# Performance work log

Measured on AMD Instinct MI355X. Metric: run time of the kernel, lower is better.

The kernel has to match this reference:

```python
import jax, jax.numpy as jnp
import numpy as np

B, S, D, H = 4, 2048, 1024, 16
HD = D // H

def setup_inputs() -> dict:
    key = jax.random.key(0)
    ks = jax.random.split(key, 5)
    x = jax.random.normal(ks[0], (B, S, D), dtype=jnp.float32)
    mask = jnp.ones((B, S), dtype=jnp.int32)
    # torch nn.Linear init scale ~ 1/sqrt(fan_in); use small normal for stability
    qkv_w = jax.random.normal(ks[1], (3 * D, D), dtype=jnp.float32) * (1.0 / np.sqrt(D))
    qkv_b = jax.random.normal(ks[2], (3 * D,), dtype=jnp.float32) * 0.02
    out_w = jax.random.normal(ks[3], (D, D), dtype=jnp.float32) * (1.0 / np.sqrt(D))
    out_b = jax.random.normal(ks[4], (D,), dtype=jnp.float32) * 0.02
    return {"x": x, "mask": mask, "qkv_w": qkv_w, "qkv_b": qkv_b,
            "out_w": out_w, "out_b": out_b}

def reference(x, mask, qkv_w, qkv_b, out_w, out_b):
    b, s, d = x.shape
    scale = np.sqrt(HD).astype(np.float32)
    # qkv projection: torch Linear y = x @ W^T + b
    qkv = x @ qkv_w.T + qkv_b                      # (b, s, 3d)
    qkv = qkv.reshape(b, s, 3, H, HD)
    qkv = jnp.transpose(qkv, (2, 0, 3, 1, 4))      # (3, b, H, s, hd)
    q, k, v = qkv[0], qkv[1], qkv[2]
    scores = jnp.einsum('bhqd,bhkd->bhqk', q, k) / scale  # (b, H, s, s)
    neg_inf = jnp.float32(-jnp.inf)
    causal = jnp.tril(jnp.ones((s, s), dtype=bool))
    scores = jnp.where(causal[None, None], scores, neg_inf)
    key_mask = (mask != 0)[:, None, None, :]       # (b, 1, 1, s)
    scores = jnp.where(key_mask, scores, neg_inf)
    attn = jax.nn.softmax(scores, axis=-1)
    out = jnp.einsum('bhqk,bhkd->bhqd', attn, v)   # (b, H, s, hd)
    out = jnp.transpose(out, (0, 2, 1, 3)).reshape(b, s, d)
    return out @ out_w.T + out_b
```

## Files before the change

### kernel.cpp

```cpp
#include <hip/hip_runtime.h>
#include <stdint.h>
#include <type_traits>

#define BB  4
#define SS  2048
#define DD  1024
#define HH  16
#define HDD 64

typedef __attribute__((ext_vector_type(8))) short s16x8;
typedef __attribute__((ext_vector_type(4))) float f32x4;

__device__ inline short f2bf(float f) {
    union { float f; unsigned int u; } v; v.f = f;
    unsigned int r = (v.u + 0x7fffu + ((v.u >> 16) & 1u)) >> 16;
    return (short)r;
}

__device__ inline float bf2f(short s) {
    union { unsigned int u; float f; } v;
    v.u = ((unsigned int)(unsigned short)s) << 16;
    return v.f;
}

__device__ inline unsigned int pk2(float a, float b) {
    return (unsigned int)(unsigned short)f2bf(a) |
           ((unsigned int)(unsigned short)f2bf(b) << 16);
}

#define GLL(gp, lp) __builtin_amdgcn_global_load_lds( \
    (const __attribute__((address_space(1))) void*)(gp), \
    (__attribute__((address_space(3))) void*)(lp), 16, 0, 0)

__device__ inline void lds_barrier() {
    asm volatile("s_waitcnt lgkmcnt(0)" ::: "memory");
    __builtin_amdgcn_sched_barrier(0);
    __builtin_amdgcn_s_barrier();
    __builtin_amdgcn_sched_barrier(0);
}

__global__ void cvt_all(const float* __restrict__ x, const float* __restrict__ qw,
                        const float* __restrict__ ow, short* __restrict__ dst) {
    const int X_N  = BB * SS * DD;
    const int QW_N = 3 * DD * DD;
    int i = (blockIdx.x * 256 + threadIdx.x) * 8;
    const float* s;
    if (i < X_N)            s = x + i;
    else if (i < X_N + QW_N) s = qw + (i - X_N);
    else                     s = ow + (i - X_N - QW_N);
    const float4* sp = (const float4*)s;
    float4 a = sp[0], b = sp[1];
    s16x8 o;
    o[0]=f2bf(a.x); o[1]=f2bf(a.y); o[2]=f2bf(a.z); o[3]=f2bf(a.w);
    o[4]=f2bf(b.x); o[5]=f2bf(b.y); o[6]=f2bf(b.z); o[7]=f2bf(b.w);
    *(s16x8*)(dst + i) = o;
}

template<int EPI>
__global__ __launch_bounds__(256, 3)
void gemm128tb(const short* __restrict__ A, const short* __restrict__ Bw,
               const float* __restrict__ bias, float* __restrict__ Cf,
               short* __restrict__ Qo, short* __restrict__ Ko, short* __restrict__ Vo,
               int M, int N, int K, int nbx)
{
    __shared__ short lsA[3][128 * 32];
    __shared__ short lsB[3][128 * 32];

    const int tid  = threadIdx.x;
    const int w    = tid >> 6, lane = tid & 63;
    const int quad = lane >> 4, l15 = lane & 15;
    const int wm = w >> 1, wn = w & 1;
    const int cpx = gridDim.x >> 3;
    const int swz = (blockIdx.x & 7) * cpx + (blockIdx.x >> 3);
    const int m0 = (swz / nbx) * 128, n0 = (swz % nbx) * 128;
    const int grow = lane >> 2;
    const int gcol = ((lane & 3) ^ (grow & 3)) * 8;
    const int rsw = (l15 & 3);

    f32x4 acc[4][4] = {};

    auto issue = [&](int kt, int buf) {
#pragma unroll
        for (int jj = 0; jj < 2; ++jj) {
            int c = w * 2 + jj;
            GLL(A + (size_t)(m0 + c * 16 + grow) * K + kt * 32 + gcol,
                &lsA[buf][c * 512]);
        }
#pragma unroll
        for (int jj = 0; jj < 2; ++jj) {
            int c = w * 2 + jj;
            GLL(Bw + (size_t)(n0 + c * 16 + grow) * K + kt * 32 + gcol,
                &lsB[buf][c * 512]);
        }
    };

    const int NT = K >> 5;
    issue(0, 0);
    issue(1, 1);
    int buf = 0;
    for (int t = 0; t < NT; ++t) {
        lds_barrier();
        const int nb2 = (buf + 2 >= 3) ? buf - 1 : buf + 2;
        if (t + 2 < NT) {
            issue(t + 2, nb2);
            asm volatile("s_waitcnt vmcnt(8)" ::: "memory");
        } else if (t + 1 < NT) {
            asm volatile("s_waitcnt vmcnt(4)" ::: "memory");
        } else {
            asm volatile("s_waitcnt vmcnt(0)" ::: "memory");
        }
        __builtin_amdgcn_sched_barrier(0);
        __builtin_amdgcn_s_barrier();
        __builtin_amdgcn_sched_barrier(0);

        s16x8 af[4], bfr[4];
#pragma unroll
        for (int mf = 0; mf < 4; ++mf)
            af[mf] = *(const s16x8*)&lsA[buf][(wm * 64 + mf * 16 + l15) * 32 +
                                             ((quad ^ rsw) * 8)];
#pragma unroll
        for (int nf = 0; nf < 4; ++nf)
            bfr[nf] = *(const s16x8*)&lsB[buf][(wn * 64 + nf * 16 + l15) * 32 +
                                              ((quad ^ rsw) * 8)];

        __builtin_amdgcn_s_setprio(1);
#pragma unroll
        for (int mf = 0; mf < 4; ++mf)
#pragma unroll
            for (int nf = 0; nf < 4; ++nf)
                acc[mf][nf] = __builtin_amdgcn_mfma_f32_16x16x32_bf16(
                                  af[mf], bfr[nf], acc[mf][nf], 0, 0, 0);
        __builtin_amdgcn_s_setprio(0);

        buf = (buf + 1 >= 3) ? 0 : buf + 1;
    }

    if (EPI == 0) {
#pragma unroll
        for (int mf = 0; mf < 4; ++mf) {
            int row = m0 + wm * 64 + mf * 16 + quad * 4;
#pragma unroll
            for (int nf = 0; nf < 4; ++nf) {
                int col = n0 + wn * 64 + nf * 16 + l15;
                float bv = bias[col];
#pragma unroll
                for (int r = 0; r < 4; ++r)
                    Cf[(size_t)(row + r) * N + col] = acc[mf][nf][r] + bv;
            }
        }
    } else {
#pragma unroll
        for (int mf = 0; mf < 4; ++mf) {
            int row = m0 + wm * 64 + mf * 16 + quad * 4;
#pragma unroll
            for (int nf = 0; nf < 4; ++nf) {
                int col = n0 + wn * 64 + nf * 16 + l15;
                float bv = bias[col];
                int sel = col >> 10, h = (col >> 6) & 15, hd = col & 63;
#pragma unroll
                for (int r = 0; r < 4; ++r) {
                    int rr = row + r;
                    int b = rr >> 11, s = rr & 2047;
                    short val = f2bf(acc[mf][nf][r] + bv);
                    if (sel == 0)      Qo[(((size_t)b * HH + h) * SS + s) * HDD + hd] = val;
                    else if (sel == 1) Ko[(((size_t)b * HH + h) * SS + s) * HDD + hd] = val;
                    else               Vo[(((size_t)b * HH + h) * HDD + hd) * SS + s] = val;
                }
            }
        }
    }
}

__global__ __launch_bounds__(256, 2)
void attn_kernel(const short* __restrict__ Q, const short* __restrict__ Kb,
                 const short* __restrict__ Vb, const int* __restrict__ mask,
                 short* __restrict__ O)
{
    __shared__ short lsK[2][64 * 64];
    __shared__ short lsV[2][64 * 64];
    __shared__ short lsP[4][32 * 64];
    __shared__ short lsM[SS];

    const int tid  = threadIdx.x;
    const int w    = tid >> 6, lane = tid & 63;
    const int quad = lane >> 4, l15 = lane & 15;
    const int L  = blockIdx.x + 8 * blockIdx.y;
    const int bx = L >> 6;
    const int bh = (L & 7) * 8 + ((L >> 3) & 7);
    const int b = bh >> 4;
    const size_t baseQK = (size_t)bh * SS * HDD;
    const size_t baseV  = (size_t)bh * HDD * SS;
    const float SC = 0.18033688f;
    const int grow = lane >> 3;
    const int gcol = ((lane & 7) ^ grow) * 8;
    const int l7 = l15 & 7;

    {
        const int4* mp = (const int4*)(mask + b * SS);
        int4 a = mp[tid * 2], c = mp[tid * 2 + 1];
        const short NEG = f2bf(-1e30f);
        s16x8 mo;
        mo[0] = a.x ? (short)0 : NEG; mo[1] = a.y ? (short)0 : NEG;
        mo[2] = a.z ? (short)0 : NEG; mo[3] = a.w ? (short)0 : NEG;
        mo[4] = c.x ? (short)0 : NEG; mo[5] = c.y ? (short)0 : NEG;
        mo[6] = c.z ? (short)0 : NEG; mo[7] = c.w ? (short)0 : NEG;
        *(s16x8*)&lsM[tid * 8] = mo;
    }

    auto issue = [&](int kv0, int buf) {
#pragma unroll
        for (int jj = 0; jj < 2; ++jj) {
            int row = w * 16 + jj * 8 + grow;
            GLL(Kb + baseQK + (size_t)(kv0 + row) * HDD + gcol,
                &lsK[buf][(w * 2 + jj) * 512]);
        }
#pragma unroll
        for (int jj = 0; jj < 2; ++jj) {
            int row = w * 16 + jj * 8 + grow;
            GLL(Vb + baseV + (size_t)row * SS + kv0 + gcol,
                &lsV[buf][(w * 2 + jj) * 512]);
        }
    };

    for (int t = 0; t < 2; ++t) {
        const int qb = t ? bx : (15 - bx);
        const int q0 = qb * 128;
        const int qw0 = q0 + w * 32;

        s16x8 aq[2][2];
#pragma unroll
        for (int s = 0; s < 2; ++s)
#pragma unroll
            for (int ks = 0; ks < 2; ++ks)
                aq[s][ks] = *(const s16x8*)(Q + baseQK +
                    (size_t)(qw0 + s * 16 + l15) * HDD + ks * 32 + quad * 8);

        float m_r[2], l_r[2];
        f32x4 o_acc[2][4] = {};
#pragma unroll
        for (int s = 0; s < 2; ++s) { m_r[s] = -1e30f; l_r[s] = 0.f; }

        const int ntiles = 2 * qb + 2;

        lds_barrier();
        issue(0, 0);

        auto tile = [&](auto CC, int kv0, int buf, int kvn) {
            constexpr bool CAUS = decltype(CC)::value;

            lds_barrier();
            if (kvn >= 0) issue(kvn, buf ^ 1);

            float madd[4][4];
#pragma unroll
            for (int nt = 0; nt < 4; ++nt) {
                uint2 mw4 = *(const uint2*)&lsM[kv0 + nt * 16 + quad * 4];
                madd[nt][0] = bf2f((short)(mw4.x & 0xffff));
                madd[nt][1] = bf2f((short)(mw4.x >> 16));
                madd[nt][2] = bf2f((short)(mw4.y & 0xffff));
                madd[nt][3] = bf2f((short)(mw4.y >> 16));
            }

            if (kvn >= 0) asm volatile("s_waitcnt vmcnt(4)" ::: "memory");
            else          asm volatile("s_waitcnt vmcnt(0)" ::: "memory");
            __builtin_amdgcn_sched_barrier(0);
            __builtin_amdgcn_s_barrier();
            __builtin_amdgcn_sched_barrier(0);

            f32x4 sv[2][4];
#pragma unroll
            for (int s = 0; s < 2; ++s)
#pragma unroll
                for (int nt = 0; nt < 4; ++nt) sv[s][nt] = f32x4{};
#pragma unroll
            for (int ks = 0; ks < 2; ++ks)
#pragma unroll
                for (int nt = 0; nt < 4; ++nt) {
                    s16x8 kf = *(const s16x8*)&lsK[buf][(nt * 16 + l15) * 64 +
                                                       (((ks * 4 + quad) ^ l7) * 8)];
#pragma unroll
                    for (int s = 0; s < 2; ++s)
                        sv[s][nt] = __builtin_amdgcn_mfma_f32_16x16x32_bf16(
                                        kf, aq[s][ks], sv[s][nt], 0, 0, 0);
                }

#pragma unroll
            for (int s = 0; s < 2; ++s) {
                const int qg = qw0 + s * 16 + l15;
#pragma unroll
                for (int nt = 0; nt < 4; ++nt) {
                    const int kg0 = kv0 + nt * 16 + quad * 4;
#pragma unroll
                    for (int r = 0; r < 4; ++r) {
                        float scv = sv[s][nt][r] * SC + madd[nt][r];
                        if (CAUS && kg0 + r > qg) scv = -1e30f;
                        sv[s][nt][r] = scv;
                    }
                }
            }

            float rm[2];
#pragma unroll
            for (int s = 0; s < 2; ++s) {
                float v = fmaxf(fmaxf(fmaxf(sv[s][0][0], sv[s][0][1]),
                                      fmaxf(sv[s][0][2], sv[s][0][3])),
                                fmaxf(fmaxf(sv[s][1][0], sv[s][1][1]),
                                      fmaxf(sv[s][1][2], sv[s][1][3])));
                float v2 = fmaxf(fmaxf(fmaxf(sv[s][2][0], sv[s][2][1]),
                                       fmaxf(sv[s][2][2], sv[s][2][3])),
                                 fmaxf(fmaxf(sv[s][3][0], sv[s][3][1]),
                                       fmaxf(sv[s][3][2], sv[s][3][3])));
                v = fmaxf(v, v2);
                v = fmaxf(v, __shfl_xor(v, 16));
                v = fmaxf(v, __shfl_xor(v, 32));
                rm[s] = v;
            }
            float need = fmaxf(rm[0] - m_r[0], rm[1] - m_r[1]);
            if (!__all(need <= 8.0f)) {
#pragma unroll
                for (int s = 0; s < 2; ++s) {
                    float nm = fmaxf(m_r[s], rm[s]);
                    float al = __builtin_amdgcn_exp2f(m_r[s] - nm);
                    m_r[s] = nm;
                    l_r[s] *= al;
#pragma unroll
                    for (int r = 0; r < 4; ++r) {
                        float alq = __shfl(al, (quad << 2) + r + (lane & 48));
#pragma unroll
                        for (int ht = 0; ht < 4; ++ht)
                            o_acc[s][ht][r] *= alq;
                    }
                }
            }
#pragma unroll
            for (int s = 0; s < 2; ++s) {
                float rs = 0.f;
#pragma unroll
                for (int nt = 0; nt < 4; ++nt)
#pragma unroll
                    for (int r = 0; r < 4; ++r) {
                        float p = __builtin_amdgcn_exp2f(sv[s][nt][r] - m_r[s]);
                        sv[s][nt][r] = p;
                        rs += p;
                    }
                l_r[s] += rs;
            }

            short* lsPw = lsP[w];
#pragma unroll
            for (int s = 0; s < 2; ++s)
#pragma unroll
                for (int nt = 0; nt < 4; ++nt) {
                    uint2 pw;
                    pw.x = pk2(sv[s][nt][0], sv[s][nt][1]);
                    pw.y = pk2(sv[s][nt][2], sv[s][nt][3]);
                    int row = s * 16 + l15;
                    int g8 = (nt * 2 + (quad >> 1)) ^ l7;
                    *(uint2*)&lsPw[row * 64 + (g8 << 3) + ((quad & 1) << 2)] = pw;
                }
            asm volatile("s_waitcnt lgkmcnt(0)" ::: "memory");
            __builtin_amdgcn_sched_barrier(0);

            s16x8 ap[2][2];
#pragma unroll
            for (int s = 0; s < 2; ++s)
#pragma unroll
                for (int k2 = 0; k2 < 2; ++k2)
                    ap[s][k2] = *(const s16x8*)&lsPw[(s * 16 + l15) * 64 +
                                                     (((k2 * 4 + quad) ^ l7) << 3)];
#pragma unroll
            for (int ht = 0; ht < 4; ++ht)
#pragma unroll
                for (int k2 = 0; k2 < 2; ++k2) {
                    s16x8 vf = *(const s16x8*)&lsV[buf][(ht * 16 + l15) * 64 +
                                                        (((k2 * 4 + quad) ^ l7) * 8)];
#pragma unroll
                    for (int s = 0; s < 2; ++s)
                        o_acc[s][ht] = __builtin_amdgcn_mfma_f32_16x16x32_bf16(
                                           ap[s][k2], vf, o_acc[s][ht], 0, 0, 0);
                }
        };

        for (int kt = 0; kt < ntiles; ++kt) {
            const int kvn = (kt + 1 < ntiles) ? (kt + 1) * 64 : -1;
            if (kt >= 2 * qb) tile(std::true_type{},  kt * 64, kt & 1, kvn);
            else              tile(std::false_type{}, kt * 64, kt & 1, kvn);
        }

        const int hcol = (bh & 15) * HDD;
#pragma unroll
        for (int s = 0; s < 2; ++s) {
            float ls = l_r[s];
            ls += __shfl_xor(ls, 16);
            ls += __shfl_xor(ls, 32);
#pragma unroll
            for (int r = 0; r < 4; ++r) {
                float lq = __shfl(ls, (quad << 2) + r + (lane & 48));
                float inv = 1.0f / lq;
                int srow = qw0 + s * 16 + quad * 4 + r;
                size_t base = ((size_t)b * SS + srow) * DD + hcol;
#pragma unroll
                for (int ht = 0; ht < 4; ++ht)
                    O[base + ht * 16 + l15] = f2bf(o_acc[s][ht][r] * inv);
            }
        }
    }
}

extern "C" void kernel_launch(void* const* d_in, const int* in_sizes, int n_in,
                              void* d_out, int out_size, void* d_ws, size_t ws_size,
                              hipStream_t stream) {
    const float* x     = (const float*)d_in[0];
    const int*   mask  = (const int*)d_in[1];
    const float* qkv_w = (const float*)d_in[2];
    const float* qkv_b = (const float*)d_in[3];
    const float* out_w = (const float*)d_in[4];
    const float* out_b = (const float*)d_in[5];
    float* out = (float*)d_out;

    const size_t M1 = (size_t)BB * SS;
    short* ws  = (short*)d_ws;
    short* xb  = ws;
    short* qwb = xb  + M1 * DD;
    short* owb = qwb + (size_t)3 * DD * DD;
    short* Qb  = owb + (size_t)DD * DD;
    short* Kb  = Qb  + M1 * DD;
    short* Vb  = Kb  + M1 * DD;
    short* Ob  = Vb  + M1 * DD;

    cvt_all<<<6144, 256, 0, stream>>>(x, qkv_w, out_w, ws);

    gemm128tb<1><<<1536, 256, 0, stream>>>(xb, qwb, qkv_b, nullptr,
                                           Qb, Kb, Vb, 8192, 3072, 1024, 24);
    attn_kernel<<<dim3(8, BB * HH), 256, 0, stream>>>(Qb, Kb, Vb, mask, Ob);
    gemm128tb<0><<<512, 256, 0, stream>>>(Ob, owb, out_b, out,
                                          nullptr, nullptr, nullptr, 8192, 1024, 1024, 8);
}
```

Before: 284.4 us.

## Double KV tile size to 128 and read mask directly from global memory

The attention kernel now processes 128 keys per tile instead of 64. This halves the number of tile iterations and their barriers and softmax rescale checks per query block. LDS buffers for K and V grow to match, and the V tile uses a new swizzle for the 128-wide rows. The shared-memory mask staging is removed in favour of per-tile int4 loads from global memory, which saves LDS and an init pass but adds global loads in each tile. The larger S fragments raise register pressure and LDS use, which may reduce occupancy at two blocks per SM.

```diff
diff --git a/kernel.cpp b/kernel.cpp
--- a/kernel.cpp
+++ b/kernel.cpp
@@ -15,12 +15,6 @@
     union { float f; unsigned int u; } v; v.f = f;
     unsigned int r = (v.u + 0x7fffu + ((v.u >> 16) & 1u)) >> 16;
     return (short)r;
-}
-
-__device__ inline float bf2f(short s) {
-    union { unsigned int u; float f; } v;
-    v.u = ((unsigned int)(unsigned short)s) << 16;
-    return v.f;
 }
 
 __device__ inline unsigned int pk2(float a, float b) {
@@ -176,10 +170,9 @@
                  const short* __restrict__ Vb, const int* __restrict__ mask,
                  short* __restrict__ O)
 {
-    __shared__ short lsK[2][64 * 64];
-    __shared__ short lsV[2][64 * 64];
+    __shared__ short lsK[2][128 * 64];
+    __shared__ short lsV[2][64 * 128];
     __shared__ short lsP[4][32 * 64];
-    __shared__ short lsM[SS];
 
     const int tid  = threadIdx.x;
     const int w    = tid >> 6, lane = tid & 63;
@@ -194,31 +187,22 @@
     const int grow = lane >> 3;
     const int gcol = ((lane & 7) ^ grow) * 8;
     const int l7 = l15 & 7;
-
-    {
-        const int4* mp = (const int4*)(mask + b * SS);
-        int4 a = mp[tid * 2], c = mp[tid * 2 + 1];
-        const short NEG = f2bf(-1e30f);
-        s16x8 mo;
-        mo[0] = a.x ? (short)0 : NEG; mo[1] = a.y ? (short)0 : NEG;
-        mo[2] = a.z ? (short)0 : NEG; mo[3] = a.w ? (short)0 : NEG;
-        mo[4] = c.x ? (short)0 : NEG; mo[5] = c.y ? (short)0 : NEG;
-        mo[6] = c.z ? (short)0 : NEG; mo[7] = c.w ? (short)0 : NEG;
-        *(s16x8*)&lsM[tid * 8] = mo;
-    }
+    const int vrow_in = lane >> 4;
 
     auto issue = [&](int kv0, int buf) {
 #pragma unroll
-        for (int jj = 0; jj < 2; ++jj) {
-            int row = w * 16 + jj * 8 + grow;
-            GLL(Kb + baseQK + (size_t)(kv0 + row) * HDD + gcol,
-                &lsK[buf][(w * 2 + jj) * 512]);
-        }
-#pragma unroll
-        for (int jj = 0; jj < 2; ++jj) {
-            int row = w * 16 + jj * 8 + grow;
-            GLL(Vb + baseV + (size_t)row * SS + kv0 + gcol,
-                &lsV[buf][(w * 2 + jj) * 512]);
+        for (int jj = 0; jj < 4; ++jj) {
+            int c = w * 4 + jj;
+            GLL(Kb + baseQK + (size_t)(kv0 + c * 8 + grow) * HDD + gcol,
+                &lsK[buf][c * 512]);
+        }
+#pragma unroll
+        for (int jj = 0; jj < 4; ++jj) {
+            int c = w * 4 + jj;
+            int vrow = c * 4 + vrow_in;
+            int vg = (lane & 15) ^ (vrow & 7);
+            GLL(Vb + baseV + (size_t)vrow * SS + kv0 + vg * 8,
+                &lsV[buf][c * 512]);
         }
     };
 
@@ -240,7 +224,7 @@
 #pragma unroll
         for (int s = 0; s < 2; ++s) { m_r[s] = -1e30f; l_r[s] = 0.f; }
 
-        const int ntiles = 2 * qb + 2;
+        const int ntiles = qb + 1;
 
         lds_barrier();
         issue(0, 0);
@@ -249,33 +233,34 @@
             constexpr bool CAUS = decltype(CC)::value;
 
             lds_barrier();
+
+            float madd[8][4];
+#pragma unroll
+            for (int nt = 0; nt < 8; ++nt) {
+                int4 mi = *(const int4*)(mask + b * SS + kv0 + nt * 16 + quad * 4);
+                madd[nt][0] = mi.x ? 0.f : -1e30f;
+                madd[nt][1] = mi.y ? 0.f : -1e30f;
+                madd[nt][2] = mi.z ? 0.f : -1e30f;
+                madd[nt][3] = mi.w ? 0.f : -1e30f;
+            }
+            __builtin_amdgcn_sched_barrier(0);
             if (kvn >= 0) issue(kvn, buf ^ 1);
 
-            float madd[4][4];
-#pragma unroll
-            for (int nt = 0; nt < 4; ++nt) {
-                uint2 mw4 = *(const uint2*)&lsM[kv0 + nt * 16 + quad * 4];
-                madd[nt][0] = bf2f((short)(mw4.x & 0xffff));
-                madd[nt][1] = bf2f((short)(mw4.x >> 16));
-                madd[nt][2] = bf2f((short)(mw4.y & 0xffff));
-                madd[nt][3] = bf2f((short)(mw4.y >> 16));
-            }
-
-            if (kvn >= 0) asm volatile("s_waitcnt vmcnt(4)" ::: "memory");
+            if (kvn >= 0) asm volatile("s_waitcnt vmcnt(8)" ::: "memory");
             else          asm volatile("s_waitcnt vmcnt(0)" ::: "memory");
             __builtin_amdgcn_sched_barrier(0);
             __builtin_amdgcn_s_barrier();
             __builtin_amdgcn_sched_barrier(0);
 
-            f32x4 sv[2][4];
+            f32x4 sv[2][8];
 #pragma unroll
             for (int s = 0; s < 2; ++s)
 #pragma unroll
-                for (int nt = 0; nt < 4; ++nt) sv[s][nt] = f32x4{};
+                for (int nt = 0; nt < 8; ++nt) sv[s][nt] = f32x4{};
 #pragma unroll
             for (int ks = 0; ks < 2; ++ks)
 #pragma unroll
-                for (int nt = 0; nt < 4; ++nt) {
+                for (int nt = 0; nt < 8; ++nt) {
                     s16x8 kf = *(const s16x8*)&lsK[buf][(nt * 16 + l15) * 64 +
                                                        (((ks * 4 + quad) ^ l7) * 8)];
 #pragma unroll
@@ -288,7 +273,7 @@
             for (int s = 0; s < 2; ++s) {
                 const int qg = qw0 + s * 16 + l15;
 #pragma unroll
-                for (int nt = 0; nt < 4; ++nt) {
+                for (int nt = 0; nt < 8; ++nt) {
                     const int kg0 = kv0 + nt * 16 + quad * 4;
 #pragma unroll
                     for (int r = 0; r < 4; ++r) {
@@ -302,15 +287,11 @@
             float rm[2];
 #pragma unroll
             for (int s = 0; s < 2; ++s) {
-                float v = fmaxf(fmaxf(fmaxf(sv[s][0][0], sv[s][0][1]),
-                                      fmaxf(sv[s][0][2], sv[s][0][3])),
-                                fmaxf(fmaxf(sv[s][1][0], sv[s][1][1]),
-                                      fmaxf(sv[s][1][2], sv[s][1][3])));
-                float v2 = fmaxf(fmaxf(fmaxf(sv[s][2][0], sv[s][2][1]),
-                                       fmaxf(sv[s][2][2], sv[s][2][3])),
-                                 fmaxf(fmaxf(sv[s][3][0], sv[s][3][1]),
-                                       fmaxf(sv[s][3][2], sv[s][3][3])));
-                v = fmaxf(v, v2);
+                float v = -1e30f;
+#pragma unroll
+                for (int nt = 0; nt < 8; ++nt)
+                    v = fmaxf(v, fmaxf(fmaxf(sv[s][nt][0], sv[s][nt][1]),
+                                       fmaxf(sv[s][nt][2], sv[s][nt][3])));
                 v = fmaxf(v, __shfl_xor(v, 16));
                 v = fmaxf(v, __shfl_xor(v, 32));
                 rm[s] = v;
@@ -336,7 +317,7 @@
             for (int s = 0; s < 2; ++s) {
                 float rs = 0.f;
 #pragma unroll
-                for (int nt = 0; nt < 4; ++nt)
+                for (int nt = 0; nt < 8; ++nt)
 #pragma unroll
                     for (int r = 0; r < 4; ++r) {
                         float p = __builtin_amdgcn_exp2f(sv[s][nt][r] - m_r[s]);
@@ -348,43 +329,47 @@
 
             short* lsPw = lsP[w];
 #pragma unroll
-            for (int s = 0; s < 2; ++s)
-#pragma unroll
-                for (int nt = 0; nt < 4; ++nt) {
-                    uint2 pw;
-                    pw.x = pk2(sv[s][nt][0], sv[s][nt][1]);
-                    pw.y = pk2(sv[s][nt][2], sv[s][nt][3]);
-                    int row = s * 16 + l15;
-                    int g8 = (nt * 2 + (quad >> 1)) ^ l7;
-                    *(uint2*)&lsPw[row * 64 + (g8 << 3) + ((quad & 1) << 2)] = pw;
-                }
-            asm volatile("s_waitcnt lgkmcnt(0)" ::: "memory");
-            __builtin_amdgcn_sched_barrier(0);
-
-            s16x8 ap[2][2];
-#pragma unroll
-            for (int s = 0; s < 2; ++s)
-#pragma unroll
-                for (int k2 = 0; k2 < 2; ++k2)
-                    ap[s][k2] = *(const s16x8*)&lsPw[(s * 16 + l15) * 64 +
-                                                     (((k2 * 4 + quad) ^ l7) << 3)];
-#pragma unroll
-            for (int ht = 0; ht < 4; ++ht)
-#pragma unroll
-                for (int k2 = 0; k2 < 2; ++k2) {
-                    s16x8 vf = *(const s16x8*)&lsV[buf][(ht * 16 + l15) * 64 +
-                                                        (((k2 * 4 + quad) ^ l7) * 8)];
-#pragma unroll
-                    for (int s = 0; s < 2; ++s)
-                        o_acc[s][ht] = __builtin_amdgcn_mfma_f32_16x16x32_bf16(
-                                           ap[s][k2], vf, o_acc[s][ht], 0, 0, 0);
-                }
+            for (int half = 0; half < 2; ++half) {
+#pragma unroll
+                for (int s = 0; s < 2; ++s)
+#pragma unroll
+                    for (int nt2 = 0; nt2 < 4; ++nt2) {
+                        int nt = half * 4 + nt2;
+                        uint2 pw;
+                        pw.x = pk2(sv[s][nt][0], sv[s][nt][1]);
+                        pw.y = pk2(sv[s][nt][2], sv[s][nt][3]);
+                        int row = s * 16 + l15;
+                        int g8 = (nt2 * 2 + (quad >> 1)) ^ l7;
+                        *(uint2*)&lsPw[row * 64 + (g8 << 3) + ((quad & 1) << 2)] = pw;
+                    }
+                asm volatile("s_waitcnt lgkmcnt(0)" ::: "memory");
+                __builtin_amdgcn_sched_barrier(0);
+
+                s16x8 ap[2][2];
+#pragma unroll
+                for (int s = 0; s < 2; ++s)
+#pragma unroll
+                    for (int k2 = 0; k2 < 2; ++k2)
+                        ap[s][k2] = *(const s16x8*)&lsPw[(s * 16 + l15) * 64 +
+                                                         (((k2 * 4 + quad) ^ l7) << 3)];
+#pragma unroll
+                for (int ht = 0; ht < 4; ++ht)
+#pragma unroll
+                    for (int k2 = 0; k2 < 2; ++k2) {
+                        s16x8 vf = *(const s16x8*)&lsV[buf][(ht * 16 + l15) * 128 +
+                                        (((half * 8 + k2 * 4 + quad) ^ l7) * 8)];
+#pragma unroll
+                        for (int s = 0; s < 2; ++s)
+                            o_acc[s][ht] = __builtin_amdgcn_mfma_f32_16x16x32_bf16(
+                                               ap[s][k2], vf, o_acc[s][ht], 0, 0, 0);
+                    }
+            }
         };
 
         for (int kt = 0; kt < ntiles; ++kt) {
-            const int kvn = (kt + 1 < ntiles) ? (kt + 1) * 64 : -1;
-            if (kt >= 2 * qb) tile(std::true_type{},  kt * 64, kt & 1, kvn);
-            else              tile(std::false_type{}, kt * 64, kt & 1, kvn);
+            const int kvn = (kt + 1 < ntiles) ? (kt + 1) * 128 : -1;
+            if (kt == ntiles - 1) tile(std::true_type{},  kt * 128, kt & 1, kvn);
+            else                  tile(std::false_type{}, kt * 128, kt & 1, kvn);
         }
 
         const int hcol = (bh & 15) * HDD;
```

Result: no change. 287.8 us (+1.2%).
